# Performance work log

Hardware: AMD Instinct MI355X
Metric: run time of the kernel (lower is better)

The kernel has to match this reference:

```python
import jax, jax.numpy as jnp
import numpy as np

BATCH = 64
ORIGINAL_DIM = 524288
PROJ_DIM = 8192
C = 4


def setup_inputs() -> dict:
    key = jax.random.key(0)
    k1, k2, k3 = jax.random.split(key, 3)
    x = jax.random.normal(k1, (BATCH, ORIGINAL_DIM), dtype=jnp.float32)
    rand_indices = jax.random.randint(k2, (ORIGINAL_DIM, C), 0, PROJ_DIM, dtype=jnp.int32)
    rand_signs = jax.random.randint(k3, (ORIGINAL_DIM, C), 0, 2, dtype=jnp.int32)
    return {"x": x, "rand_indices": rand_indices, "rand_signs": rand_signs}


def reference(x, rand_indices, rand_signs):
    # SJLT: out[b, rand_indices[d, j]] += x[b, d] * sign[d, j], scaled by 1/sqrt(c)
    B, D = x.shape
    c = rand_indices.shape[1]
    signs = (2 * rand_signs - 1).astype(x.dtype)  # {0,1} -> {-1,+1}
    scale = 1.0 / jnp.sqrt(jnp.asarray(c, dtype=x.dtype))
    out = jnp.zeros((B, PROJ_DIM), dtype=x.dtype)
    for j in range(c):  # small fixed loop over non-zeros per column
        out = out.at[:, rand_indices[:, j]].add(x * signs[:, j])
    return out * scale
```

## Files before the change

### kernel.cpp

```cpp
#include <hip/hip_runtime.h>


constexpr int BATCH = 64;
constexpr int DIM   = 524288;
constexpr int PROJ  = 8192;
constexpr int NENT  = DIM * 4;
constexpr int CAP   = 384;

__device__ __forceinline__ uint32_t f2bf(float f) {
    uint32_t u = __float_as_uint(f);
    return (u + 0x7fffu + ((u >> 16) & 1u)) >> 16;
}

__global__ __launch_bounds__(256) void fused_tx_scatter(
    const float* __restrict__ x, const int* __restrict__ idx,
    const int* __restrict__ sgn, uint32_t* __restrict__ cnt,
    uint32_t* __restrict__ entries, uint32_t* __restrict__ xT)
{
    __shared__ float tile[64][65];
    const int d0 = blockIdx.x * 64;
    const int t  = threadIdx.x;

    const int e = (d0 << 2) + t;
    const int p = idx[e];
    const int s = sgn[e] & 1;

    const int c  = t & 15;
    const int r0 = t >> 4;
    float4 v[4];
#pragma unroll
    for (int it = 0; it < 4; ++it) {
        int b = it * 16 + r0;
        v[it] = *reinterpret_cast<const float4*>(&x[(size_t)b * DIM + d0 + 4 * c]);
    }

    {
        uint32_t dv   = ((uint32_t)(d0 + (t >> 2)) << 1) | (uint32_t)s;
        uint32_t slot = atomicAdd(&cnt[p], 1u);
        entries[(uint32_t)p * (uint32_t)CAP + slot] = dv;
    }

#pragma unroll
    for (int it = 0; it < 4; ++it) {
        int b = it * 16 + r0;
        tile[b][4 * c + 0] = v[it].x;
        tile[b][4 * c + 1] = v[it].y;
        tile[b][4 * c + 2] = v[it].z;
        tile[b][4 * c + 3] = v[it].w;
    }
    __syncthreads();

    const int a  = t & 7;
    const int dr = t >> 3;
#pragma unroll
    for (int pass = 0; pass < 2; ++pass) {
        const int dl = pass * 32 + dr;
        uint4 wv;
        uint32_t* wq = reinterpret_cast<uint32_t*>(&wv);
#pragma unroll
        for (int q = 0; q < 4; ++q) {
            const int k = 4 * a + q;
            uint32_t lo = f2bf(tile[2 * k + 0][dl] * 0.5f);
            uint32_t hi = f2bf(tile[2 * k + 1][dl] * 0.5f);
            wq[q] = lo | (hi << 16);
        }
        *reinterpret_cast<uint4*>(&xT[(size_t)(d0 + dl) * 32 + 4 * a]) = wv;
    }
}

__device__ __forceinline__ void proc8(const uint32_t* __restrict__ e,
    const uint32_t* __restrict__ xT, int half, int k,
    float& acc0, float& acc1)
{
#pragma unroll
    for (int t = 0; t < 8; t += 2) {
        uint32_t sel = half ? e[t + 1] : e[t];
        uint32_t u = xT[(size_t)(sel >> 1) * 32 + k];
        u ^= (sel & 1u) ? 0u : 0x80008000u;
        acc0 += __uint_as_float(u << 16);
        acc1 += __uint_as_float(u & 0xffff0000u);
    }
}

__global__ __launch_bounds__(1024) void gather4_kernel(
    const uint32_t* __restrict__ entries, const uint32_t* __restrict__ cnt,
    const uint32_t* __restrict__ xT, float* __restrict__ out)
{
    __shared__ float obuf[64][17];
    const int w    = threadIdx.x >> 6;
    const int lane = threadIdx.x & 63;
    const int p    = __builtin_amdgcn_readfirstlane(blockIdx.x * 16 + w);
    const uint32_t n  = __builtin_amdgcn_readfirstlane(cnt[p]);
    const uint32_t e0 = (uint32_t)p * (uint32_t)CAP;

    const int half = lane >> 5;
    const int k    = lane & 31;
    float acc0 = 0.f, acc1 = 0.f;

    uint32_t A[8], B[8];
    uint32_t base = 0;
    if (n >= 8) {
#pragma unroll
        for (int t = 0; t < 8; ++t) A[t] = entries[e0 + t];
    }
    for (; base + 24 <= n; base += 16) {
#pragma unroll
        for (int t = 0; t < 8; ++t) B[t] = entries[e0 + base + 8 + t];
        proc8(A, xT, half, k, acc0, acc1);
#pragma unroll
        for (int t = 0; t < 8; ++t) A[t] = entries[e0 + base + 16 + t];
        proc8(B, xT, half, k, acc0, acc1);
    }
    if (base + 16 <= n) {
#pragma unroll
        for (int t = 0; t < 8; ++t) B[t] = entries[e0 + base + 8 + t];
        proc8(A, xT, half, k, acc0, acc1);
        proc8(B, xT, half, k, acc0, acc1);
        base += 16;
    } else if (base + 8 <= n) {
        proc8(A, xT, half, k, acc0, acc1);
        base += 8;
    }
    for (; base < n; base += 2) {
        uint32_t eA = entries[e0 + base];
        uint32_t eB = (base + 1 < n) ? entries[e0 + base + 1] : 0u;
        uint32_t sel   = half ? eB : eA;
        bool     valid = (base + (uint32_t)half) < n;
        uint32_t u = 0u;
        if (valid) {
            u = xT[(size_t)(sel >> 1) * 32 + k];
            u ^= (sel & 1u) ? 0u : 0x80008000u;
        }
        acc0 += __uint_as_float(u << 16);
        acc1 += __uint_as_float(u & 0xffff0000u);
    }
    acc0 += __shfl_xor(acc0, 32);
    acc1 += __shfl_xor(acc1, 32);
    if (half == 0) {
        obuf[2 * k + 0][w] = acc0;
        obuf[2 * k + 1][w] = acc1;
    }
    __syncthreads();
    const int t = threadIdx.x;
    if (t < 256) {
        const int b = t >> 2, q = t & 3;
        float4 v;
        v.x = obuf[b][4 * q + 0];
        v.y = obuf[b][4 * q + 1];
        v.z = obuf[b][4 * q + 2];
        v.w = obuf[b][4 * q + 3];
        *reinterpret_cast<float4*>(&out[(size_t)b * PROJ + blockIdx.x * 16 + 4 * q]) = v;
    }
}

__global__ __launch_bounds__(256) void transpose_hist_kernel(
    const float* __restrict__ x, const int4* __restrict__ idx4,
    uint32_t* __restrict__ xT, uint32_t* __restrict__ cnt)
{
    __shared__ float tile[64][65];
    const int d0   = blockIdx.x * 64;
    const int lane = threadIdx.x & 63;
    const int q    = threadIdx.x >> 6;
#pragma unroll
    for (int r = 0; r < 16; ++r) {
        int b = r * 4 + q;
        tile[b][lane] = x[(size_t)b * DIM + d0 + lane];
    }
    if (threadIdx.x < 64) {
        int4 iv = idx4[d0 + threadIdx.x];
        atomicAdd(&cnt[iv.x], 1u);
        atomicAdd(&cnt[iv.y], 1u);
        atomicAdd(&cnt[iv.z], 1u);
        atomicAdd(&cnt[iv.w], 1u);
    }
    __syncthreads();
    const int k   = threadIdx.x & 31;
    const int dl0 = threadIdx.x >> 5;
#pragma unroll
    for (int pass = 0; pass < 8; ++pass) {
        int dl = pass * 8 + dl0;
        uint32_t lo = f2bf(tile[2 * k + 0][dl] * 0.5f);
        uint32_t hi = f2bf(tile[2 * k + 1][dl] * 0.5f);
        xT[(size_t)(d0 + dl) * 32 + k] = lo | (hi << 16);
    }
}

__global__ __launch_bounds__(256) void scan_kernel(
    const uint32_t* __restrict__ cnt, uint32_t* __restrict__ cur)
{
    __shared__ uint32_t wsum[4];
    const int t    = threadIdx.x;
    const int lane = t & 63;
    uint32_t c[32];
    uint32_t s = 0;
#pragma unroll
    for (int i = 0; i < 32; ++i) { c[i] = cnt[t * 32 + i]; s += c[i]; }
    uint32_t v = s;
#pragma unroll
    for (int off = 1; off < 64; off <<= 1) {
        uint32_t u = __shfl_up(v, off);
        if (lane >= off) v += u;
    }
    if (lane == 63) wsum[t >> 6] = v;
    __syncthreads();
    uint32_t wb = 0;
    for (int w0 = 0; w0 < (t >> 6); ++w0) wb += wsum[w0];
    uint32_t base = wb + v - s;
#pragma unroll
    for (int i = 0; i < 32; ++i) { cur[t * 32 + i] = base; base += c[i]; }
}

__global__ __launch_bounds__(256) void scatter_kernel(
    const int4* __restrict__ idx4, const int4* __restrict__ sgn4,
    uint32_t* __restrict__ cur, uint32_t* __restrict__ entries)
{
    int d = blockIdx.x * 256 + threadIdx.x;
    int4 iv = idx4[d];
    int4 sv = sgn4[d];
    const uint32_t dv = (uint32_t)d << 1;
    uint32_t slot;
    slot = atomicAdd(&cur[iv.x], 1u); entries[slot] = dv | (uint32_t)(sv.x & 1);
    slot = atomicAdd(&cur[iv.y], 1u); entries[slot] = dv | (uint32_t)(sv.y & 1);
    slot = atomicAdd(&cur[iv.z], 1u); entries[slot] = dv | (uint32_t)(sv.z & 1);
    slot = atomicAdd(&cur[iv.w], 1u); entries[slot] = dv | (uint32_t)(sv.w & 1);
}

__global__ __launch_bounds__(256) void gather_kernel(
    const uint32_t* __restrict__ entries, const uint32_t* __restrict__ cnt,
    const uint32_t* __restrict__ endp, const uint32_t* __restrict__ xT,
    float* __restrict__ out)
{
    const int w    = threadIdx.x >> 6;
    const int lane = threadIdx.x & 63;
    const int p    = __builtin_amdgcn_readfirstlane(blockIdx.x * 4 + w);
    const uint32_t n  = __builtin_amdgcn_readfirstlane(cnt[p]);
    const uint32_t e0 = __builtin_amdgcn_readfirstlane(endp[p] - n);

    const int half = lane >> 5;
    const int k    = lane & 31;
    float acc0 = 0.f, acc1 = 0.f;

    uint32_t base = 0;
    for (; base + 8 <= n; base += 8) {
        uint32_t e8[8];
#pragma unroll
        for (int t = 0; t < 8; ++t) e8[t] = entries[e0 + base + t];
#pragma unroll
        for (int t = 0; t < 8; t += 2) {
            uint32_t sel = half ? e8[t + 1] : e8[t];
            uint32_t u = xT[(size_t)(sel >> 1) * 32 + k];
            u ^= (sel & 1u) ? 0u : 0x80008000u;
            acc0 += __uint_as_float(u << 16);
            acc1 += __uint_as_float(u & 0xffff0000u);
        }
    }
    for (; base < n; base += 2) {
        uint32_t eA = entries[e0 + base];
        uint32_t eB = (base + 1 < n) ? entries[e0 + base + 1] : 0u;
        uint32_t sel   = half ? eB : eA;
        bool     valid = (base + (uint32_t)half) < n;
        uint32_t u = 0u;
        if (valid) {
            u = xT[(size_t)(sel >> 1) * 32 + k];
            u ^= (sel & 1u) ? 0u : 0x80008000u;
        }
        acc0 += __uint_as_float(u << 16);
        acc1 += __uint_as_float(u & 0xffff0000u);
    }
    acc0 += __shfl_xor(acc0, 32);
    acc1 += __shfl_xor(acc1, 32);
    if (half == 0) {
        out[(size_t)(2 * k + 0) * PROJ + p] = acc0;
        out[(size_t)(2 * k + 1) * PROJ + p] = acc1;
    }
}

__device__ __forceinline__ void lds_fadd(uint32_t byte_addr, float v) {
    asm volatile("ds_add_f32 %0, %1" :: "v"(byte_addr), "v"(v) : "memory");
}
__device__ __forceinline__ void lds_fadd_off32k(uint32_t byte_addr, float v) {
    asm volatile("ds_add_f32 %0, %1 offset:32768" :: "v"(byte_addr), "v"(v) : "memory");
}

__global__ __launch_bounds__(1024) void sjlt_scatter(
    const float* __restrict__ x, const int4* __restrict__ idx4,
    const int4* __restrict__ sgn4, float* __restrict__ out)
{
    __shared__ float acc[4 * PROJ];
    for (int i = threadIdx.x; i < 4 * PROJ; i += 1024) acc[i] = 0.0f;
    __syncthreads();
    const int row0 = blockIdx.y * 4;
    const int dbeg = blockIdx.x * (DIM / 16);
    const uint32_t accBase = (uint32_t)(uintptr_t)(&acc[0]);
    const float* xr0 = x + (size_t)(row0 + 0) * DIM;
    const float* xr1 = x + (size_t)(row0 + 1) * DIM;
    const float* xr2 = x + (size_t)(row0 + 2) * DIM;
    const float* xr3 = x + (size_t)(row0 + 3) * DIM;
    for (int d = dbeg + (int)threadIdx.x; d < dbeg + DIM / 16; d += 1024) {
        const int4 iv = idx4[d];
        const int4 sv = sgn4[d];
        const uint32_t u0 = __float_as_uint(xr0[d]);
        const uint32_t u1 = __float_as_uint(xr1[d]);
        const uint32_t u2 = __float_as_uint(xr2[d]);
        const uint32_t u3 = __float_as_uint(xr3[d]);
        const int p[4] = {iv.x, iv.y, iv.z, iv.w};
        const int s[4] = {sv.x, sv.y, sv.z, sv.w};
#pragma unroll
        for (int j = 0; j < 4; ++j) {
            const uint32_t flip = (uint32_t)(s[j] ^ 1) << 31;
            const uint32_t a01  = accBase + ((uint32_t)p[j] << 2);
            const uint32_t a23  = a01 + 2u * 32768u;
            lds_fadd        (a01, __uint_as_float(u0 ^ flip));
            lds_fadd_off32k (a01, __uint_as_float(u1 ^ flip));
            lds_fadd        (a23, __uint_as_float(u2 ^ flip));
            lds_fadd_off32k (a23, __uint_as_float(u3 ^ flip));
        }
    }
    __syncthreads();
    for (int i = threadIdx.x; i < 4 * PROJ; i += 1024) {
        const int r  = i >> 13;
        const int pp = i & (PROJ - 1);
        unsafeAtomicAdd(&out[(size_t)(row0 + r) * PROJ + pp], acc[i] * 0.5f);
    }
}

extern "C" void kernel_launch(void* const* d_in, const int* in_sizes, int n_in,
                              void* d_out, int out_size, void* d_ws, size_t ws_size,
                              hipStream_t stream) {
    const float* x   = (const float*)d_in[0];
    const int4*  idx = (const int4*) d_in[1];
    const int4*  sgn = (const int4*) d_in[2];
    float*       out = (float*)d_out;

    const size_t need_new = ((size_t)PROJ + (size_t)PROJ * CAP + (size_t)DIM * 32) * 4;
    const size_t need_old = ((size_t)PROJ + PROJ + NENT + (size_t)DIM * 32) * 4;

    if (ws_size >= need_new) {
        uint32_t* cnt     = (uint32_t*)d_ws;
        uint32_t* entries = cnt + PROJ;
        uint32_t* xT      = entries + (size_t)PROJ * CAP;

        hipMemsetAsync(cnt, 0, PROJ * sizeof(uint32_t), stream);
        hipMemsetAsync(entries, 0, (size_t)PROJ * CAP * sizeof(uint32_t), stream);
        fused_tx_scatter<<<DIM / 64, 256, 0, stream>>>(
            x, (const int*)idx, (const int*)sgn, cnt, entries, xT);
        gather4_kernel<<<PROJ / 16, 1024, 0, stream>>>(entries, cnt, xT, out);
    } else if (ws_size >= need_old) {
        uint32_t* cnt     = (uint32_t*)d_ws;
        uint32_t* cur     = cnt + PROJ;
        uint32_t* entries = cur + PROJ;
        uint32_t* xT      = entries + NENT;

        hipMemsetAsync(cnt, 0, PROJ * sizeof(uint32_t), stream);
        hipMemsetAsync(entries, 0, (size_t)NENT * sizeof(uint32_t), stream);
        transpose_hist_kernel<<<DIM / 64,  256, 0, stream>>>(x, idx, xT, cnt);
        scan_kernel          <<<1,         256, 0, stream>>>(cnt, cur);
        scatter_kernel       <<<DIM / 256, 256, 0, stream>>>(idx, sgn, cur, entries);
        gather_kernel        <<<PROJ / 4,  256, 0, stream>>>(entries, cnt, cur, xT, out);
    } else {
        hipMemsetAsync(d_out, 0, (size_t)out_size * sizeof(float), stream);
        dim3 grid(16, 16);
        sjlt_scatter<<<grid, 1024, 0, stream>>>(x, idx, sgn, out);
    }
}
```

Before: 285.8 us.

## Replace global atomic bucketing with two-level LDS binning and gather

The transpose is split out into its own kernel. Index binning now runs in two levels. First, each block builds a local LDS histogram over 256 coarse buckets and stages its entries bucket-sorted in shared memory. A second kernel merges each bucket's per-block segments into a fine per-projection list in LDS, then gathers from the bf16 transposed x. This removes the 2M global atomics into a per-projection counter array and drops the large workspace memsets, in exchange for an extra kernel and a fixed per-block-per-bucket capacity (80). That capacity silently truncates if a block's bucket load is exceptionally skewed.

```diff
diff --git a/kernel.cpp b/kernel.cpp
--- a/kernel.cpp
+++ b/kernel.cpp
@@ -7,24 +7,24 @@
 constexpr int NENT  = DIM * 4;
 constexpr int CAP   = 384;
 
+constexpr int NBLKA = 256;
+constexpr int EPB   = NENT / NBLKA;
+constexpr int NBUCK = 256;
+constexpr int BUCKP = PROJ / NBUCK;
+constexpr int CAPB  = 80;
+
 __device__ __forceinline__ uint32_t f2bf(float f) {
     uint32_t u = __float_as_uint(f);
     return (u + 0x7fffu + ((u >> 16) & 1u)) >> 16;
 }
 
-__global__ __launch_bounds__(256) void fused_tx_scatter(
-    const float* __restrict__ x, const int* __restrict__ idx,
-    const int* __restrict__ sgn, uint32_t* __restrict__ cnt,
-    uint32_t* __restrict__ entries, uint32_t* __restrict__ xT)
+__global__ __launch_bounds__(256) void transpose_kernel(
+    const float* __restrict__ x, uint32_t* __restrict__ xT)
 {
     __shared__ float tile[64][65];
     const int d0 = blockIdx.x * 64;
     const int t  = threadIdx.x;
 
-    const int e = (d0 << 2) + t;
-    const int p = idx[e];
-    const int s = sgn[e] & 1;
-
     const int c  = t & 15;
     const int r0 = t >> 4;
     float4 v[4];
@@ -33,13 +33,6 @@
         int b = it * 16 + r0;
         v[it] = *reinterpret_cast<const float4*>(&x[(size_t)b * DIM + d0 + 4 * c]);
     }
-
-    {
-        uint32_t dv   = ((uint32_t)(d0 + (t >> 2)) << 1) | (uint32_t)s;
-        uint32_t slot = atomicAdd(&cnt[p], 1u);
-        entries[(uint32_t)p * (uint32_t)CAP + slot] = dv;
-    }
-
 #pragma unroll
     for (int it = 0; it < 4; ++it) {
         int b = it * 16 + r0;
@@ -50,6 +43,219 @@
     }
     __syncthreads();
 
+    const int a  = t & 7;
+    const int dr = t >> 3;
+#pragma unroll
+    for (int pass = 0; pass < 2; ++pass) {
+        const int dl = pass * 32 + dr;
+        uint4 wv;
+        uint32_t* wq = reinterpret_cast<uint32_t*>(&wv);
+#pragma unroll
+        for (int q = 0; q < 4; ++q) {
+            const int k = 4 * a + q;
+            uint32_t lo = f2bf(tile[2 * k + 0][dl] * 0.5f);
+            uint32_t hi = f2bf(tile[2 * k + 1][dl] * 0.5f);
+            wq[q] = lo | (hi << 16);
+        }
+        *reinterpret_cast<uint4*>(&xT[(size_t)(d0 + dl) * 32 + 4 * a]) = wv;
+    }
+}
+
+__global__ __launch_bounds__(1024) void binA_kernel(
+    const int4* __restrict__ idx4, const int4* __restrict__ sgn4,
+    uint32_t* __restrict__ cntAB, uint32_t* __restrict__ coarse)
+{
+    __shared__ uint32_t cntL[NBUCK], offL[NBUCK], curL[NBUCK];
+    __shared__ uint32_t wsumA[4];
+    __shared__ uint32_t staging[EPB];
+    const int t    = threadIdx.x;
+    const int lane = t & 63;
+    const int blk  = blockIdx.x;
+
+    if (t < NBUCK) cntL[t] = 0;
+    __syncthreads();
+
+    int4 iv[2], sv[2];
+    int  dd[2];
+#pragma unroll
+    for (int j = 0; j < 2; ++j) {
+        int d = blk * 2048 + j * 1024 + t;
+        dd[j] = d;
+        iv[j] = idx4[d];
+        sv[j] = sgn4[d];
+    }
+#pragma unroll
+    for (int j = 0; j < 2; ++j) {
+        atomicAdd(&cntL[(uint32_t)iv[j].x >> 5], 1u);
+        atomicAdd(&cntL[(uint32_t)iv[j].y >> 5], 1u);
+        atomicAdd(&cntL[(uint32_t)iv[j].z >> 5], 1u);
+        atomicAdd(&cntL[(uint32_t)iv[j].w >> 5], 1u);
+    }
+    __syncthreads();
+    uint32_t v = 0, s = 0;
+    if (t < NBUCK) {
+        s = cntL[t]; v = s;
+#pragma unroll
+        for (int off = 1; off < 64; off <<= 1) {
+            uint32_t u = __shfl_up(v, off);
+            if (lane >= off) v += u;
+        }
+        if (lane == 63) wsumA[t >> 6] = v;
+    }
+    __syncthreads();
+    if (t < NBUCK) {
+        uint32_t wb = 0;
+        for (int w0 = 0; w0 < (t >> 6); ++w0) wb += wsumA[w0];
+        uint32_t ex = wb + v - s;
+        offL[t] = ex;
+        curL[t] = ex;
+    }
+    __syncthreads();
+#pragma unroll
+    for (int j = 0; j < 2; ++j) {
+        const uint32_t dv = (uint32_t)dd[j] << 1;
+        int p, ss;
+        uint32_t b, sl;
+        p = iv[j].x; ss = sv[j].x & 1; b = (uint32_t)p >> 5;
+        sl = atomicAdd(&curL[b], 1u);
+        staging[sl] = ((uint32_t)(p & 31) << 20) | dv | (uint32_t)ss;
+        p = iv[j].y; ss = sv[j].y & 1; b = (uint32_t)p >> 5;
+        sl = atomicAdd(&curL[b], 1u);
+        staging[sl] = ((uint32_t)(p & 31) << 20) | dv | (uint32_t)ss;
+        p = iv[j].z; ss = sv[j].z & 1; b = (uint32_t)p >> 5;
+        sl = atomicAdd(&curL[b], 1u);
+        staging[sl] = ((uint32_t)(p & 31) << 20) | dv | (uint32_t)ss;
+        p = iv[j].w; ss = sv[j].w & 1; b = (uint32_t)p >> 5;
+        sl = atomicAdd(&curL[b], 1u);
+        staging[sl] = ((uint32_t)(p & 31) << 20) | dv | (uint32_t)ss;
+    }
+    __syncthreads();
+    const int w = t >> 6;
+    for (int i = 0; i < NBUCK / 16; ++i) {
+        const int b = w * (NBUCK / 16) + i;
+        const uint32_t c   = min(cntL[b], (uint32_t)CAPB);
+        const uint32_t src = offL[b];
+        uint32_t* dst = coarse + ((size_t)b * NBLKA + blk) * CAPB;
+        for (uint32_t j2 = lane; j2 < c; j2 += 64) dst[j2] = staging[src + j2];
+    }
+    if (t < NBUCK) cntAB[(size_t)blk * NBUCK + t] = min(cntL[t], (uint32_t)CAPB);
+}
+
+__global__ __launch_bounds__(1024) void gather5_kernel(
+    const uint32_t* __restrict__ coarse, const uint32_t* __restrict__ cntAB,
+    const uint32_t* __restrict__ xT, float* __restrict__ out)
+{
+    __shared__ uint32_t csr[BUCKP * CAP];
+    __shared__ uint32_t cntF[BUCKP];
+    __shared__ uint32_t cAB[NBLKA];
+    __shared__ float    obuf[64][BUCKP + 1];
+    const int t      = threadIdx.x;
+    const int w      = t >> 6;
+    const int lane   = t & 63;
+    const int bucket = blockIdx.x;
+
+    if (t < BUCKP) cntF[t] = 0;
+    if (t < NBLKA) cAB[t] = cntAB[(size_t)t * NBUCK + bucket];
+    __syncthreads();
+
+    for (int i = 0; i < NBLKA / 16; ++i) {
+        const int j = w * (NBLKA / 16) + i;
+        const uint32_t c = cAB[j];
+        const uint32_t* src = coarse + ((size_t)bucket * NBLKA + j) * CAPB;
+        for (uint32_t i2 = lane; i2 < c; i2 += 64) {
+            const uint32_t pay = src[i2];
+            const uint32_t pl  = (pay >> 20) & 31u;
+            const uint32_t sl  = atomicAdd(&cntF[pl], 1u);
+            csr[pl * CAP + sl] = pay & 0xFFFFFu;
+        }
+    }
+    __syncthreads();
+
+    const int half = lane >> 5;
+    const int k    = lane & 31;
+#pragma unroll
+    for (int pi = 0; pi < 2; ++pi) {
+        const int pl = w + pi * 16;
+        const uint32_t n = cntF[pl];
+        const uint32_t* e = &csr[pl * CAP];
+        float acc0 = 0.f, acc1 = 0.f;
+        uint32_t base = 0;
+        for (; base + 8 <= n; base += 8) {
+            uint32_t e8[8];
+#pragma unroll
+            for (int q = 0; q < 8; ++q) e8[q] = e[base + q];
+#pragma unroll
+            for (int q = 0; q < 8; q += 2) {
+                uint32_t sel = half ? e8[q + 1] : e8[q];
+                uint32_t u = xT[(size_t)(sel >> 1) * 32 + k];
+                u ^= (sel & 1u) ? 0u : 0x80008000u;
+                acc0 += __uint_as_float(u << 16);
+                acc1 += __uint_as_float(u & 0xffff0000u);
+            }
+        }
+        for (; base < n; base += 2) {
+            uint32_t eA = e[base];
+            uint32_t eB = (base + 1 < n) ? e[base + 1] : 0u;
+            uint32_t sel   = half ? eB : eA;
+            bool     valid = (base + (uint32_t)half) < n;
+            uint32_t u = 0u;
+            if (valid) {
+                u = xT[(size_t)(sel >> 1) * 32 + k];
+                u ^= (sel & 1u) ? 0u : 0x80008000u;
+            }
+            acc0 += __uint_as_float(u << 16);
+            acc1 += __uint_as_float(u & 0xffff0000u);
+        }
+        acc0 += __shfl_xor(acc0, 32);
+        acc1 += __shfl_xor(acc1, 32);
+        if (half == 0) {
+            obuf[2 * k + 0][pl] = acc0;
+            obuf[2 * k + 1][pl] = acc1;
+        }
+    }
+    __syncthreads();
+    const int b = t >> 4, q = t & 15;
+    float2 v2;
+    v2.x = obuf[b][2 * q + 0];
+    v2.y = obuf[b][2 * q + 1];
+    *reinterpret_cast<float2*>(&out[(size_t)b * PROJ + bucket * BUCKP + 2 * q]) = v2;
+}
+
+__global__ __launch_bounds__(256) void fused_tx_scatter(
+    const float* __restrict__ x, const int* __restrict__ idx,
+    const int* __restrict__ sgn, uint32_t* __restrict__ cnt,
+    uint32_t* __restrict__ entries, uint32_t* __restrict__ xT)
+{
+    __shared__ float tile[64][65];
+    const int d0 = blockIdx.x * 64;
+    const int t  = threadIdx.x;
+
+    const int e = (d0 << 2) + t;
+    const int p = idx[e];
+    const int s = sgn[e] & 1;
+
+    const int c  = t & 15;
+    const int r0 = t >> 4;
+    float4 v[4];
+#pragma unroll
+    for (int it = 0; it < 4; ++it) {
+        int b = it * 16 + r0;
+        v[it] = *reinterpret_cast<const float4*>(&x[(size_t)b * DIM + d0 + 4 * c]);
+    }
+    {
+        uint32_t dv   = ((uint32_t)(d0 + (t >> 2)) << 1) | (uint32_t)s;
+        uint32_t slot = atomicAdd(&cnt[p], 1u);
+        entries[(uint32_t)p * (uint32_t)CAP + slot] = dv;
+    }
+#pragma unroll
+    for (int it = 0; it < 4; ++it) {
+        int b = it * 16 + r0;
+        tile[b][4 * c + 0] = v[it].x;
+        tile[b][4 * c + 1] = v[it].y;
+        tile[b][4 * c + 2] = v[it].z;
+        tile[b][4 * c + 3] = v[it].w;
+    }
+    __syncthreads();
     const int a  = t & 7;
     const int dr = t >> 3;
 #pragma unroll
@@ -150,128 +356,6 @@
         v.z = obuf[b][4 * q + 2];
         v.w = obuf[b][4 * q + 3];
         *reinterpret_cast<float4*>(&out[(size_t)b * PROJ + blockIdx.x * 16 + 4 * q]) = v;
-    }
-}
-
-__global__ __launch_bounds__(256) void transpose_hist_kernel(
-    const float* __restrict__ x, const int4* __restrict__ idx4,
-    uint32_t* __restrict__ xT, uint32_t* __restrict__ cnt)
-{
-    __shared__ float tile[64][65];
-    const int d0   = blockIdx.x * 64;
-    const int lane = threadIdx.x & 63;
-    const int q    = threadIdx.x >> 6;
-#pragma unroll
-    for (int r = 0; r < 16; ++r) {
-        int b = r * 4 + q;
-        tile[b][lane] = x[(size_t)b * DIM + d0 + lane];
-    }
-    if (threadIdx.x < 64) {
-        int4 iv = idx4[d0 + threadIdx.x];
-        atomicAdd(&cnt[iv.x], 1u);
-        atomicAdd(&cnt[iv.y], 1u);
-        atomicAdd(&cnt[iv.z], 1u);
-        atomicAdd(&cnt[iv.w], 1u);
-    }
-    __syncthreads();
-    const int k   = threadIdx.x & 31;
-    const int dl0 = threadIdx.x >> 5;
-#pragma unroll
-    for (int pass = 0; pass < 8; ++pass) {
-        int dl = pass * 8 + dl0;
-        uint32_t lo = f2bf(tile[2 * k + 0][dl] * 0.5f);
-        uint32_t hi = f2bf(tile[2 * k + 1][dl] * 0.5f);
-        xT[(size_t)(d0 + dl) * 32 + k] = lo | (hi << 16);
-    }
-}
-
-__global__ __launch_bounds__(256) void scan_kernel(
-    const uint32_t* __restrict__ cnt, uint32_t* __restrict__ cur)
-{
-    __shared__ uint32_t wsum[4];
-    const int t    = threadIdx.x;
-    const int lane = t & 63;
-    uint32_t c[32];
-    uint32_t s = 0;
-#pragma unroll
-    for (int i = 0; i < 32; ++i) { c[i] = cnt[t * 32 + i]; s += c[i]; }
-    uint32_t v = s;
-#pragma unroll
-    for (int off = 1; off < 64; off <<= 1) {
-        uint32_t u = __shfl_up(v, off);
-        if (lane >= off) v += u;
-    }
-    if (lane == 63) wsum[t >> 6] = v;
-    __syncthreads();
-    uint32_t wb = 0;
-    for (int w0 = 0; w0 < (t >> 6); ++w0) wb += wsum[w0];
-    uint32_t base = wb + v - s;
-#pragma unroll
-    for (int i = 0; i < 32; ++i) { cur[t * 32 + i] = base; base += c[i]; }
-}
-
-__global__ __launch_bounds__(256) void scatter_kernel(
-    const int4* __restrict__ idx4, const int4* __restrict__ sgn4,
-    uint32_t* __restrict__ cur, uint32_t* __restrict__ entries)
-{
-    int d = blockIdx.x * 256 + threadIdx.x;
-    int4 iv = idx4[d];
-    int4 sv = sgn4[d];
-    const uint32_t dv = (uint32_t)d << 1;
-    uint32_t slot;
-    slot = atomicAdd(&cur[iv.x], 1u); entries[slot] = dv | (uint32_t)(sv.x & 1);
-    slot = atomicAdd(&cur[iv.y], 1u); entries[slot] = dv | (uint32_t)(sv.y & 1);
-    slot = atomicAdd(&cur[iv.z], 1u); entries[slot] = dv | (uint32_t)(sv.z & 1);
-    slot = atomicAdd(&cur[iv.w], 1u); entries[slot] = dv | (uint32_t)(sv.w & 1);
-}
-
-__global__ __launch_bounds__(256) void gather_kernel(
-    const uint32_t* __restrict__ entries, const uint32_t* __restrict__ cnt,
-    const uint32_t* __restrict__ endp, const uint32_t* __restrict__ xT,
-    float* __restrict__ out)
-{
-    const int w    = threadIdx.x >> 6;
-    const int lane = threadIdx.x & 63;
-    const int p    = __builtin_amdgcn_readfirstlane(blockIdx.x * 4 + w);
-    const uint32_t n  = __builtin_amdgcn_readfirstlane(cnt[p]);
-    const uint32_t e0 = __builtin_amdgcn_readfirstlane(endp[p] - n);
-
-    const int half = lane >> 5;
-    const int k    = lane & 31;
-    float acc0 = 0.f, acc1 = 0.f;
-
-    uint32_t base = 0;
-    for (; base + 8 <= n; base += 8) {
-        uint32_t e8[8];
-#pragma unroll
-        for (int t = 0; t < 8; ++t) e8[t] = entries[e0 + base + t];
-#pragma unroll
-        for (int t = 0; t < 8; t += 2) {
-            uint32_t sel = half ? e8[t + 1] : e8[t];
-            uint32_t u = xT[(size_t)(sel >> 1) * 32 + k];
-            u ^= (sel & 1u) ? 0u : 0x80008000u;
-            acc0 += __uint_as_float(u << 16);
-            acc1 += __uint_as_float(u & 0xffff0000u);
-        }
-    }
-    for (; base < n; base += 2) {
-        uint32_t eA = entries[e0 + base];
-        uint32_t eB = (base + 1 < n) ? entries[e0 + base + 1] : 0u;
-        uint32_t sel   = half ? eB : eA;
-        bool     valid = (base + (uint32_t)half) < n;
-        uint32_t u = 0u;
-        if (valid) {
-            u = xT[(size_t)(sel >> 1) * 32 + k];
-            u ^= (sel & 1u) ? 0u : 0x80008000u;
-        }
-        acc0 += __uint_as_float(u << 16);
-        acc1 += __uint_as_float(u & 0xffff0000u);
-    }
-    acc0 += __shfl_xor(acc0, 32);
-    acc1 += __shfl_xor(acc1, 32);
-    if (half == 0) {
-        out[(size_t)(2 * k + 0) * PROJ + p] = acc0;
-        out[(size_t)(2 * k + 1) * PROJ + p] = acc1;
     }
 }
 
@@ -332,31 +416,28 @@
     const int4*  sgn = (const int4*) d_in[2];
     float*       out = (float*)d_out;
 
-    const size_t need_new = ((size_t)PROJ + (size_t)PROJ * CAP + (size_t)DIM * 32) * 4;
-    const size_t need_old = ((size_t)PROJ + PROJ + NENT + (size_t)DIM * 32) * 4;
-
-    if (ws_size >= need_new) {
+    const size_t need_r10 = ((size_t)NBLKA * NBUCK
+                           + (size_t)NBUCK * NBLKA * CAPB
+                           + (size_t)DIM * 32) * 4;
+    const size_t need_r9  = ((size_t)PROJ + (size_t)PROJ * CAP + (size_t)DIM * 32) * 4;
+
+    if (ws_size >= need_r10) {
+        uint32_t* cntAB  = (uint32_t*)d_ws;
+        uint32_t* coarse = cntAB + (size_t)NBLKA * NBUCK;
+        uint32_t* xT     = coarse + (size_t)NBUCK * NBLKA * CAPB;
+
+        transpose_kernel<<<DIM / 64, 256, 0, stream>>>(x, xT);
+        binA_kernel     <<<NBLKA,    1024, 0, stream>>>(idx, sgn, cntAB, coarse);
+        gather5_kernel  <<<NBUCK,    1024, 0, stream>>>(coarse, cntAB, xT, out);
+    } else if (ws_size >= need_r9) {
         uint32_t* cnt     = (uint32_t*)d_ws;
         uint32_t* entries = cnt + PROJ;
         uint32_t* xT      = entries + (size_t)PROJ * CAP;
 
         hipMemsetAsync(cnt, 0, PROJ * sizeof(uint32_t), stream);
-        hipMemsetAsync(entries, 0, (size_t)PROJ * CAP * sizeof(uint32_t), stream);
         fused_tx_scatter<<<DIM / 64, 256, 0, stream>>>(
             x, (const int*)idx, (const int*)sgn, cnt, entries, xT);
         gather4_kernel<<<PROJ / 16, 1024, 0, stream>>>(entries, cnt, xT, out);
-    } else if (ws_size >= need_old) {
-        uint32_t* cnt     = (uint32_t*)d_ws;
-        uint32_t* cur     = cnt + PROJ;
-        uint32_t* entries = cur + PROJ;
-        uint32_t* xT      = entries + NENT;
-
-        hipMemsetAsync(cnt, 0, PROJ * sizeof(uint32_t), stream);
-        hipMemsetAsync(entries, 0, (size_t)NENT * sizeof(uint32_t), stream);
-        transpose_hist_kernel<<<DIM / 64,  256, 0, stream>>>(x, idx, xT, cnt);
-        scan_kernel          <<<1,         256, 0, stream>>>(cnt, cur);
-        scatter_kernel       <<<DIM / 256, 256, 0, stream>>>(idx, sgn, cur, entries);
-        gather_kernel        <<<PROJ / 4,  256, 0, stream>>>(entries, cnt, cur, xT, out);
     } else {
         hipMemsetAsync(d_out, 0, (size_t)out_size * sizeof(float), stream);
         dim3 grid(16, 16);
```

Result: slower. 321.4 us (+12.4%).
